# Optimization experiments

Hardware: AMD Instinct MI355X
Metric: run time of the kernel (lower is better)

## Reference

```python
import jax, jax.numpy as jnp
import numpy as np

D_MODEL = 512
D_AUX = 64
B, N = 8, 2048


def setup_inputs() -> dict:
    key = jax.random.key(0)
    ks = jax.random.split(key, 12)
    lim = 1.0 / np.sqrt(D_MODEL)  # torch Linear default init scale
    inp = {
        "x": jax.random.normal(ks[0], (B, N, D_MODEL), dtype=jnp.float32),
        "query_aux": jax.random.normal(ks[1], (B, N, D_AUX), dtype=jnp.float32),
        "key_aux": jax.random.normal(ks[2], (B, N, D_AUX), dtype=jnp.float32),
        "adjacency_mask": jax.random.randint(ks[3], (B, N, N), 0, 2, dtype=jnp.int32),
        "merge_coefficients": jnp.float32(0.3),
        "Wq": jax.random.uniform(ks[4], (D_MODEL, D_MODEL), jnp.float32, -lim, lim),
        "bq": jax.random.uniform(ks[5], (D_MODEL,), jnp.float32, -lim, lim),
        "Wk": jax.random.uniform(ks[6], (D_MODEL, D_MODEL), jnp.float32, -lim, lim),
        "bk": jax.random.uniform(ks[7], (D_MODEL,), jnp.float32, -lim, lim),
        "Wv": jax.random.uniform(ks[8], (D_MODEL, D_MODEL), jnp.float32, -lim, lim),
        "bv": jax.random.uniform(ks[9], (D_MODEL,), jnp.float32, -lim, lim),
        "threshold": jnp.float32(0.5),
    }
    return inp


def reference(x, query_aux, key_aux, adjacency_mask, merge_coefficients,
              Wq, bq, Wk, bk, Wv, bv, threshold):
    d_model = x.shape[-1]
    d_aux = key_aux.shape[-1]
    scale = jnp.asarray(d_model, x.dtype) ** 0.5
    scale_aux = jnp.asarray(d_aux, x.dtype) ** 0.5

    q = x @ Wq.T + bq  # [B,N,D]
    k = x @ Wk.T + bk
    v = x @ Wv.T + bv

    scores = jnp.einsum('bnd,bmd->bnm', q, k) / scale  # [B,N,N]
    scores_aux = jnp.einsum('bnd,bmd->bnm', query_aux, key_aux) / scale_aux

    # data-dependent merge: where aux score nonzero AND score above learned threshold
    merge_mask = (scores_aux != 0) & (scores > threshold)
    merged = (1.0 - merge_coefficients) * scores + merge_coefficients * scores_aux
    scores = jnp.where(merge_mask, merged, scores)

    mask_value = jnp.finfo(scores.dtype).min
    scores = jnp.where(adjacency_mask == 0, mask_value, scores)

    weights = jax.nn.softmax(scores, axis=-1)
    return jnp.einsum('bnm,bmd->bnd', weights, v)
```

## Files before the change

### kernel.cpp

```cpp
#include <hip/hip_runtime.h>
#include <cstdint>

#define SEQ    2048
#define DM     512
#define DAUX   64

typedef _Float16 f16;
typedef __attribute__((ext_vector_type(2))) _Float16 f16x2;
typedef __attribute__((ext_vector_type(4))) _Float16 f16x4;
typedef __attribute__((ext_vector_type(8))) _Float16 f16x8;
typedef __attribute__((ext_vector_type(4))) float fx4;

__device__ __forceinline__ void g2l16(const void* g, void* l) {
  __builtin_amdgcn_global_load_lds(
      (__attribute__((address_space(1))) void*)const_cast<void*>(g),
      (__attribute__((address_space(3))) void*)l, 16, 0, 0);
}

__device__ __forceinline__ void stage64(const f16* __restrict__ g0, int stride,
                                        f16* lds, int t) {
#pragma unroll
  for (int p = 0; p < 4; ++p) {
    int L = p * 256 + t;
    int row = L >> 3;
    int jp = L & 7;
    int jl = jp ^ (row & 7);
    g2l16(g0 + (size_t)row * stride + jl * 8, lds + L * 8);
  }
}

__device__ __forceinline__ f16x8 frag64(const f16* lds, int row, int kq) {
  int jp = (kq >> 3) ^ (row & 7);
  return *(const f16x8*)(lds + row * 64 + jp * 8);
}

__device__ __forceinline__ void chunk3(const f16* Ah, const f16* Al,
                                       const f16* Bh, const f16* Bl,
                                       fx4 acc[4][4], int wm, int wn, int lane) {
  const int r15 = lane & 15;
  const int q8 = (lane >> 4) * 8;
#pragma unroll
  for (int k0 = 0; k0 < 64; k0 += 32) {
    f16x8 ah[4], al[4];
#pragma unroll
    for (int it = 0; it < 4; ++it) {
      int row = wm * 64 + it * 16 + r15;
      ah[it] = frag64(Ah, row, k0 + q8);
      al[it] = frag64(Al, row, k0 + q8);
    }
#pragma unroll
    for (int jt = 0; jt < 4; ++jt) {
      int col = wn * 64 + jt * 16 + r15;
      f16x8 bh = frag64(Bh, col, k0 + q8);
      f16x8 bl = frag64(Bl, col, k0 + q8);
#pragma unroll
      for (int it = 0; it < 4; ++it) {
        acc[it][jt] = __builtin_amdgcn_mfma_f32_16x16x32_f16(ah[it], bh, acc[it][jt], 0, 0, 0);
        acc[it][jt] = __builtin_amdgcn_mfma_f32_16x16x32_f16(ah[it], bl, acc[it][jt], 0, 0, 0);
        acc[it][jt] = __builtin_amdgcn_mfma_f32_16x16x32_f16(al[it], bh, acc[it][jt], 0, 0, 0);
      }
    }
  }
}

__device__ __forceinline__ void chunk1(const f16* A, const f16* B,
                                       fx4 acc[4][4], int wm, int wn, int lane) {
  const int r15 = lane & 15;
  const int q8 = (lane >> 4) * 8;
#pragma unroll
  for (int k0 = 0; k0 < 64; k0 += 32) {
    f16x8 a[4];
#pragma unroll
    for (int it = 0; it < 4; ++it)
      a[it] = frag64(A, wm * 64 + it * 16 + r15, k0 + q8);
#pragma unroll
    for (int jt = 0; jt < 4; ++jt) {
      f16x8 b = frag64(B, wn * 64 + jt * 16 + r15, k0 + q8);
#pragma unroll
      for (int it = 0; it < 4; ++it)
        acc[it][jt] = __builtin_amdgcn_mfma_f32_16x16x32_f16(a[it], b, acc[it][jt], 0, 0, 0);
    }
  }
}

__global__ __launch_bounds__(256) void convert_split(
    const float* __restrict__ x, const float* __restrict__ Wq,
    const float* __restrict__ Wk, const float* __restrict__ Wv,
    f16* __restrict__ xh, f16* __restrict__ xl,
    f16* __restrict__ Wh, f16* __restrict__ Wl) {
  int idx = blockIdx.x * 256 + threadIdx.x;
  const float* src; f16* dh; f16* dl; size_t off;
  if (idx < 2097152) { src = x; off = (size_t)idx; dh = xh; dl = xl; }
  else {
    int rr = idx - 2097152;
    int w = rr >> 16, o = rr & 65535;
    src = (w == 0) ? Wq : (w == 1) ? Wk : Wv;
    off = (size_t)o;
    dh = Wh + (size_t)w * 262144; dl = Wl + (size_t)w * 262144;
  }
  float4 v = ((const float4*)src)[off];
  float vv[4] = {v.x, v.y, v.z, v.w};
  f16x4 hv, lv;
#pragma unroll
  for (int i = 0; i < 4; ++i) {
    float s = vv[i] * 32.0f;
    f16 hi = (f16)s;
    hv[i] = hi;
    lv[i] = (f16)(s - (float)hi);
  }
  *(f16x4*)(dh + off * 4) = hv;
  *(f16x4*)(dl + off * 4) = lv;
}

__global__ __launch_bounds__(256) void qkv_mfma(
    const f16* __restrict__ xh, const f16* __restrict__ xl,
    const f16* __restrict__ Wh, const f16* __restrict__ Wl,
    const float* __restrict__ bq, const float* __restrict__ bk, const float* __restrict__ bv,
    f16* __restrict__ qh, f16* __restrict__ ql,
    f16* __restrict__ kh, f16* __restrict__ kl,
    f16* __restrict__ vt) {
  __shared__ __align__(16) f16 sm[32768];
  f16 *Ah = sm, *Al = sm + 8192, *Bh = sm + 16384, *Bl = sm + 24576;
  const int t = threadIdx.x;
  const int i0 = blockIdx.x * 128, j0 = blockIdx.y * 128, z = blockIdx.z;
  const f16* WhZ = Wh + (size_t)z * 262144;
  const f16* WlZ = Wl + (size_t)z * 262144;
  const int lane = t & 63, wave = t >> 6;
  const int wm = wave >> 1, wn = wave & 1;
  fx4 acc[4][4] = {};
  if (z < 2) {
    for (int d0 = 0; d0 < DM; d0 += 64) {
      __syncthreads();
      stage64(xh + (size_t)i0 * DM + d0, DM, Ah, t);
      stage64(xl + (size_t)i0 * DM + d0, DM, Al, t);
      stage64(WhZ + (size_t)j0 * DM + d0, DM, Bh, t);
      stage64(WlZ + (size_t)j0 * DM + d0, DM, Bl, t);
      __syncthreads();
      chunk3(Ah, Al, Bh, Bl, acc, wm, wn, lane);
    }
  } else {
    for (int d0 = 0; d0 < DM; d0 += 64) {
      __syncthreads();
      stage64(xh + (size_t)i0 * DM + d0, DM, Ah, t);
      stage64(WhZ + (size_t)j0 * DM + d0, DM, Bh, t);
      __syncthreads();
      chunk1(Ah, Bh, acc, wm, wn, lane);
    }
  }
  const float* bias = (z == 0) ? bq : (z == 1) ? bk : bv;
  const int q4 = (lane >> 4) * 4, r15 = lane & 15;
  if (z < 2) {
    f16* oh = z ? kh : qh;  f16* ol = z ? kl : ql;
#pragma unroll
    for (int jt = 0; jt < 4; ++jt) {
      int j = j0 + wn * 64 + jt * 16 + r15;
      float bj = bias[j];
#pragma unroll
      for (int it = 0; it < 4; ++it) {
        int ib = i0 + wm * 64 + it * 16 + q4;
#pragma unroll
        for (int g = 0; g < 4; ++g) {
          float val = acc[it][jt][g] * (1.0f / 1024.0f) + bj;
          float s = val * 32.0f;
          f16 hi = (f16)s;
          oh[(size_t)(ib + g) * DM + j] = hi;
          ol[(size_t)(ib + g) * DM + j] = (f16)(s - (float)hi);
        }
      }
    }
  } else {
#pragma unroll
    for (int jt = 0; jt < 4; ++jt) {
      int j = j0 + wn * 64 + jt * 16 + r15;
      float bj = bias[j];
#pragma unroll
      for (int it = 0; it < 4; ++it) {
        int ib = i0 + wm * 64 + it * 16 + q4;
        int bb = ib >> 11, nb = ib & 2047;
        f16x4 hv;
#pragma unroll
        for (int g = 0; g < 4; ++g)
          hv[g] = (f16)(acc[it][jt][g] * (1.0f / 1024.0f) + bj);
        *(f16x4*)(vt + ((size_t)(bb * DM + j)) * SEQ + nb) = hv;
      }
    }
  }
}

__global__ __launch_bounds__(256) void scores_mfma(
    const f16* __restrict__ qh, const f16* __restrict__ ql,
    const f16* __restrict__ kh, const f16* __restrict__ kl,
    const float* __restrict__ qa, const float* __restrict__ ka,
    const int* __restrict__ adj,
    const float* __restrict__ mc_p, const float* __restrict__ thr_p,
    f16* __restrict__ S16) {
  __shared__ __align__(16) f16 sm[32768];
  f16 *Ah = sm, *Al = sm + 8192, *Bh = sm + 16384, *Bl = sm + 24576;
  f16 *QAl = sm;
  f16 *KAl = sm + 9216;
  const int t = threadIdx.x;
  const int n0 = blockIdx.x * 128, m0 = blockIdx.y * 128, b = blockIdx.z;
  const int lane = t & 63, wave = t >> 6;
  const int wm = wave >> 1, wn = wave & 1;
  const int r15 = lane & 15, qd = lane >> 4;

  const float* QAb = qa + ((size_t)b * SEQ + n0) * DAUX;
  const float* KAb = ka + ((size_t)b * SEQ + m0) * DAUX;
#pragma unroll
  for (int p = 0; p < 4; ++p) {
    int L8 = p * 256 + t;
    int row = L8 >> 3, c8 = (L8 & 7) * 8;
    float4 u0 = *(const float4*)(QAb + (size_t)row * DAUX + c8);
    float4 u1 = *(const float4*)(QAb + (size_t)row * DAUX + c8 + 4);
    f16x8 hq = {(f16)u0.x,(f16)u0.y,(f16)u0.z,(f16)u0.w,(f16)u1.x,(f16)u1.y,(f16)u1.z,(f16)u1.w};
    *(f16x8*)(QAl + row * 72 + c8) = hq;
    float4 w0 = *(const float4*)(KAb + (size_t)row * DAUX + c8);
    float4 w1 = *(const float4*)(KAb + (size_t)row * DAUX + c8 + 4);
    f16x8 hk = {(f16)w0.x,(f16)w0.y,(f16)w0.z,(f16)w0.w,(f16)w1.x,(f16)w1.y,(f16)w1.z,(f16)w1.w};
    *(f16x8*)(KAl + row * 72 + c8) = hk;
  }
  __syncthreads();
  f16x2 sax[4][4][2];
  {
    const int q8 = qd * 8;
    f16x8 qa_f[4][2], ka_f[4][2];
#pragma unroll
    for (int it = 0; it < 4; ++it) {
      int row = wm * 64 + it * 16 + r15;
      qa_f[it][0] = *(const f16x8*)(QAl + row * 72 + q8);
      qa_f[it][1] = *(const f16x8*)(QAl + row * 72 + 32 + q8);
    }
#pragma unroll
    for (int jt = 0; jt < 4; ++jt) {
      int col = wn * 64 + jt * 16 + r15;
      ka_f[jt][0] = *(const f16x8*)(KAl + col * 72 + q8);
      ka_f[jt][1] = *(const f16x8*)(KAl + col * 72 + 32 + q8);
    }
#pragma unroll
    for (int it = 0; it < 4; ++it)
#pragma unroll
      for (int jt = 0; jt < 4; ++jt) {
        fx4 tmp = {0.f, 0.f, 0.f, 0.f};
        tmp = __builtin_amdgcn_mfma_f32_16x16x32_f16(qa_f[it][0], ka_f[jt][0], tmp, 0, 0, 0);
        tmp = __builtin_amdgcn_mfma_f32_16x16x32_f16(qa_f[it][1], ka_f[jt][1], tmp, 0, 0, 0);
        sax[it][jt][0] = f16x2{(f16)tmp[0], (f16)tmp[1]};
        sax[it][jt][1] = f16x2{(f16)tmp[2], (f16)tmp[3]};
      }
  }
  fx4 acc[4][4] = {};
  const f16* qhB = qh + ((size_t)b * SEQ + n0) * DM;
  const f16* qlB = ql + ((size_t)b * SEQ + n0) * DM;
  const f16* khB = kh + ((size_t)b * SEQ + m0) * DM;
  const f16* klB = kl + ((size_t)b * SEQ + m0) * DM;
  for (int d0 = 0; d0 < DM; d0 += 64) {
    __syncthreads();
    stage64(qhB + d0, DM, Ah, t);
    stage64(qlB + d0, DM, Al, t);
    stage64(khB + d0, DM, Bh, t);
    stage64(klB + d0, DM, Bl, t);
    __syncthreads();
    chunk3(Ah, Al, Bh, Bl, acc, wm, wn, lane);
  }
  const float mc = *mc_p, thr = *thr_p;
  const float invC = 1.0f / (1024.0f * 22.62741699796952f);
#pragma unroll
  for (int it = 0; it < 4; ++it) {
    int rowb = n0 + wm * 64 + it * 16 + qd * 4;
#pragma unroll
    for (int g = 0; g < 4; ++g) {
      size_t rbase = ((size_t)b * SEQ + rowb + g) * SEQ;
#pragma unroll
      for (int jt = 0; jt < 4; ++jt) {
        int col = m0 + wn * 64 + jt * 16 + r15;
        float s = acc[it][jt][g] * invC;
        float sa = (float)sax[it][jt][g >> 1][g & 1] * 0.125f;
        if (sa != 0.0f && s > thr) s = (1.0f - mc) * s + mc * sa;
        if (adj[rbase + col] == 0) s = -65504.0f;
        S16[rbase + col] = (f16)s;
      }
    }
  }
}

__global__ __launch_bounds__(256) void softmax_p(
    f16* __restrict__ S16, float* __restrict__ rowsum) {
  const size_t row = blockIdx.x;
  f16* Sr = S16 + row * SEQ;
  const int t = threadIdx.x;
  f16x8 v = *(const f16x8*)(Sr + t * 8);
  float vals[8];
#pragma unroll
  for (int i = 0; i < 8; ++i) vals[i] = (float)v[i];
  float m = vals[0];
#pragma unroll
  for (int i = 1; i < 8; ++i) m = fmaxf(m, vals[i]);
#pragma unroll
  for (int off = 32; off >= 1; off >>= 1) m = fmaxf(m, __shfl_down(m, off, 64));
  __shared__ float wred[4];
  __shared__ float bmax;
  const int wv = t >> 6, ln = t & 63;
  if (ln == 0) wred[wv] = m;
  __syncthreads();
  if (t == 0) bmax = fmaxf(fmaxf(wred[0], wred[1]), fmaxf(wred[2], wred[3]));
  __syncthreads();
  const float mm = bmax;
  f16x8 p16;
  float z = 0.f;
#pragma unroll
  for (int i = 0; i < 8; ++i) {
    f16 p = (f16)(__expf(vals[i] - mm) * 1024.0f);
    p16[i] = p;
    z += (float)p;
  }
#pragma unroll
  for (int off = 32; off >= 1; off >>= 1) z += __shfl_down(z, off, 64);
  __syncthreads();
  if (ln == 0) wred[wv] = z;
  __syncthreads();
  if (t == 0) rowsum[row] = wred[0] + wred[1] + wred[2] + wred[3];
  *(f16x8*)(Sr + t * 8) = p16;
}

__global__ __launch_bounds__(256) void pv_mfma(
    const f16* __restrict__ P16, const f16* __restrict__ vt,
    const float* __restrict__ rowsum, float* __restrict__ O) {
  __shared__ __align__(16) f16 sm[16384];
  f16 *Ps = sm, *Vs = sm + 8192;
  const int t = threadIdx.x;
  const int n0 = blockIdx.x * 128, d0 = blockIdx.y * 128, b = blockIdx.z;
  const int lane = t & 63, wave = t >> 6;
  const int wm = wave >> 1, wn = wave & 1;
  fx4 acc[4][4] = {};
  const f16* Pb = P16 + ((size_t)b * SEQ + n0) * SEQ;
  const f16* Vb = vt + ((size_t)b * DM + d0) * SEQ;
  for (int m0 = 0; m0 < SEQ; m0 += 64) {
    __syncthreads();
    stage64(Pb + m0, SEQ, Ps, t);
    stage64(Vb + m0, SEQ, Vs, t);
    __syncthreads();
    chunk1(Ps, Vs, acc, wm, wn, lane);
  }
  const int r15 = lane & 15, qd = lane >> 4;
#pragma unroll
  for (int it = 0; it < 4; ++it) {
    int nb = n0 + wm * 64 + it * 16 + qd * 4;
#pragma unroll
    for (int g = 0; g < 4; ++g) {
      float inv = 1.0f / rowsum[(size_t)b * SEQ + nb + g];
      size_t obase = ((size_t)b * SEQ + nb + g) * DM;
#pragma unroll
      for (int jt = 0; jt < 4; ++jt) {
        int d = d0 + wn * 64 + jt * 16 + r15;
        O[obase + d] = acc[it][jt][g] * inv;
      }
    }
  }
}

extern "C" void kernel_launch(void* const* d_in, const int* in_sizes, int n_in,
                              void* d_out, int out_size, void* d_ws, size_t ws_size,
                              hipStream_t stream) {
  const float* x   = (const float*)d_in[0];
  const float* qa  = (const float*)d_in[1];
  const float* ka  = (const float*)d_in[2];
  const int*   adj = (const int*)d_in[3];
  const float* mc  = (const float*)d_in[4];
  const float* Wq  = (const float*)d_in[5];
  const float* bq  = (const float*)d_in[6];
  const float* Wk  = (const float*)d_in[7];
  const float* bk  = (const float*)d_in[8];
  const float* Wv  = (const float*)d_in[9];
  const float* bv  = (const float*)d_in[10];
  const float* thr = (const float*)d_in[11];
  float* out = (float*)d_out;

  f16* qh  = (f16*)d_ws;
  f16* ql  = qh + 8388608;
  f16* kh  = ql + 8388608;
  f16* kl  = kh + 8388608;
  f16* vt  = kl + 8388608;
  f16* S16 = vt + 8388608;
  float* rowsum = (float*)(S16 + 33554432);
  f16* xh = S16;
  f16* xl = xh + 8388608;
  f16* Wh = xl + 8388608;
  f16* Wl = Wh + 786432;

  convert_split<<<8960, 256, 0, stream>>>(x, Wq, Wk, Wv, xh, xl, Wh, Wl);
  qkv_mfma<<<dim3(128, 4, 3), 256, 0, stream>>>(xh, xl, Wh, Wl, bq, bk, bv,
                                                qh, ql, kh, kl, vt);
  scores_mfma<<<dim3(16, 16, 8), 256, 0, stream>>>(qh, ql, kh, kl, qa, ka, adj,
                                                   mc, thr, S16);
  softmax_p<<<16384, 256, 0, stream>>>(S16, rowsum);
  pv_mfma<<<dim3(16, 4, 8), 256, 0, stream>>>(S16, vt, rowsum, out);
}
```

Measured before the change: 535.6 us.

## Switch GEMMs to 32x32x16 MFMA tiles and halve LDS K-chunks

Replaces the 16x16x32 MFMA fragments with 32x32x16 instructions in the QKV, scores and PV GEMMs, changing the accumulator layout and epilogue indexing. The split-precision GEMMs now stage 32-wide K chunks with a new swizzle, which halves shared memory per block and may allow more resident blocks. The aim is fewer LDS fragment reads per FLOP and better occupancy. The cost is twice as many sync-separated staging iterations and epilogue stores whose write patterns are less coalesced.

```diff
diff --git a/kernel.cpp b/kernel.cpp
--- a/kernel.cpp
+++ b/kernel.cpp
@@ -10,11 +10,28 @@
 typedef __attribute__((ext_vector_type(4))) _Float16 f16x4;
 typedef __attribute__((ext_vector_type(8))) _Float16 f16x8;
 typedef __attribute__((ext_vector_type(4))) float fx4;
+typedef __attribute__((ext_vector_type(16))) float fx16;
 
 __device__ __forceinline__ void g2l16(const void* g, void* l) {
   __builtin_amdgcn_global_load_lds(
       (__attribute__((address_space(1))) void*)const_cast<void*>(g),
       (__attribute__((address_space(3))) void*)l, 16, 0, 0);
+}
+
+__device__ __forceinline__ void stage32(const f16* __restrict__ g0, int stride,
+                                        f16* lds, int t) {
+#pragma unroll
+  for (int p = 0; p < 2; ++p) {
+    int L = p * 256 + t;
+    int row = L >> 2;
+    int jp = L & 3;
+    int jl = jp ^ ((row >> 1) & 3);
+    g2l16(g0 + (size_t)row * stride + jl * 8, lds + L * 8);
+  }
+}
+__device__ __forceinline__ f16x8 frag32(const f16* lds, int row, int kq) {
+  int jp = (kq >> 3) ^ ((row >> 1) & 3);
+  return *(const f16x8*)(lds + row * 32 + jp * 8);
 }
 
 __device__ __forceinline__ void stage64(const f16* __restrict__ g0, int stride,
@@ -28,57 +45,56 @@
     g2l16(g0 + (size_t)row * stride + jl * 8, lds + L * 8);
   }
 }
-
 __device__ __forceinline__ f16x8 frag64(const f16* lds, int row, int kq) {
   int jp = (kq >> 3) ^ (row & 7);
   return *(const f16x8*)(lds + row * 64 + jp * 8);
 }
 
-__device__ __forceinline__ void chunk3(const f16* Ah, const f16* Al,
-                                       const f16* Bh, const f16* Bl,
-                                       fx4 acc[4][4], int wm, int wn, int lane) {
-  const int r15 = lane & 15;
-  const int q8 = (lane >> 4) * 8;
-#pragma unroll
-  for (int k0 = 0; k0 < 64; k0 += 32) {
-    f16x8 ah[4], al[4];
-#pragma unroll
-    for (int it = 0; it < 4; ++it) {
-      int row = wm * 64 + it * 16 + r15;
-      ah[it] = frag64(Ah, row, k0 + q8);
-      al[it] = frag64(Al, row, k0 + q8);
-    }
-#pragma unroll
-    for (int jt = 0; jt < 4; ++jt) {
-      int col = wn * 64 + jt * 16 + r15;
-      f16x8 bh = frag64(Bh, col, k0 + q8);
-      f16x8 bl = frag64(Bl, col, k0 + q8);
-#pragma unroll
-      for (int it = 0; it < 4; ++it) {
-        acc[it][jt] = __builtin_amdgcn_mfma_f32_16x16x32_f16(ah[it], bh, acc[it][jt], 0, 0, 0);
-        acc[it][jt] = __builtin_amdgcn_mfma_f32_16x16x32_f16(ah[it], bl, acc[it][jt], 0, 0, 0);
-        acc[it][jt] = __builtin_amdgcn_mfma_f32_16x16x32_f16(al[it], bh, acc[it][jt], 0, 0, 0);
-      }
-    }
-  }
-}
-
-__device__ __forceinline__ void chunk1(const f16* A, const f16* B,
-                                       fx4 acc[4][4], int wm, int wn, int lane) {
-  const int r15 = lane & 15;
-  const int q8 = (lane >> 4) * 8;
-#pragma unroll
-  for (int k0 = 0; k0 < 64; k0 += 32) {
-    f16x8 a[4];
-#pragma unroll
-    for (int it = 0; it < 4; ++it)
-      a[it] = frag64(A, wm * 64 + it * 16 + r15, k0 + q8);
-#pragma unroll
-    for (int jt = 0; jt < 4; ++jt) {
-      f16x8 b = frag64(B, wn * 64 + jt * 16 + r15, k0 + q8);
-#pragma unroll
-      for (int it = 0; it < 4; ++it)
-        acc[it][jt] = __builtin_amdgcn_mfma_f32_16x16x32_f16(a[it], b, acc[it][jt], 0, 0, 0);
+__device__ __forceinline__ void chunk3_32(const f16* Ah, const f16* Al,
+                                          const f16* Bh, const f16* Bl,
+                                          fx16 acc[2][2], int wm, int wn, int lane) {
+  const int r31 = lane & 31;
+  const int kq = (lane >> 5) * 8;
+#pragma unroll
+  for (int k0 = 0; k0 < 32; k0 += 16) {
+    f16x8 ah[2], al[2];
+#pragma unroll
+    for (int it = 0; it < 2; ++it) {
+      int row = wm * 64 + it * 32 + r31;
+      ah[it] = frag32(Ah, row, k0 + kq);
+      al[it] = frag32(Al, row, k0 + kq);
+    }
+#pragma unroll
+    for (int jt = 0; jt < 2; ++jt) {
+      int col = wn * 64 + jt * 32 + r31;
+      f16x8 bh = frag32(Bh, col, k0 + kq);
+      f16x8 bl = frag32(Bl, col, k0 + kq);
+#pragma unroll
+      for (int it = 0; it < 2; ++it) {
+        acc[it][jt] = __builtin_amdgcn_mfma_f32_32x32x16_f16(ah[it], bh, acc[it][jt], 0, 0, 0);
+        acc[it][jt] = __builtin_amdgcn_mfma_f32_32x32x16_f16(ah[it], bl, acc[it][jt], 0, 0, 0);
+        acc[it][jt] = __builtin_amdgcn_mfma_f32_32x32x16_f16(al[it], bh, acc[it][jt], 0, 0, 0);
+      }
+    }
+  }
+}
+
+__device__ __forceinline__ void chunk1_64(const f16* A, const f16* B,
+                                          fx16 acc[2][2], int wm, int wn, int lane) {
+  const int r31 = lane & 31;
+  const int kq = (lane >> 5) * 8;
+#pragma unroll
+  for (int k0 = 0; k0 < 64; k0 += 16) {
+    f16x8 a[2];
+#pragma unroll
+    for (int it = 0; it < 2; ++it)
+      a[it] = frag64(A, wm * 64 + it * 32 + r31, k0 + kq);
+#pragma unroll
+    for (int jt = 0; jt < 2; ++jt) {
+      f16x8 b = frag64(B, wn * 64 + jt * 32 + r31, k0 + kq);
+#pragma unroll
+      for (int it = 0; it < 2; ++it)
+        acc[it][jt] = __builtin_amdgcn_mfma_f32_32x32x16_f16(a[it], b, acc[it][jt], 0, 0, 0);
     }
   }
 }
@@ -119,71 +135,73 @@
     f16* __restrict__ qh, f16* __restrict__ ql,
     f16* __restrict__ kh, f16* __restrict__ kl,
     f16* __restrict__ vt) {
-  __shared__ __align__(16) f16 sm[32768];
-  f16 *Ah = sm, *Al = sm + 8192, *Bh = sm + 16384, *Bl = sm + 24576;
+  __shared__ __align__(16) f16 sm[16384];
   const int t = threadIdx.x;
   const int i0 = blockIdx.x * 128, j0 = blockIdx.y * 128, z = blockIdx.z;
   const f16* WhZ = Wh + (size_t)z * 262144;
   const f16* WlZ = Wl + (size_t)z * 262144;
   const int lane = t & 63, wave = t >> 6;
   const int wm = wave >> 1, wn = wave & 1;
-  fx4 acc[4][4] = {};
+  const int r31 = lane & 31, half = lane >> 5;
+  fx16 acc[2][2] = {};
   if (z < 2) {
-    for (int d0 = 0; d0 < DM; d0 += 64) {
+    f16 *Ah = sm, *Al = sm + 4096, *Bh = sm + 8192, *Bl = sm + 12288;
+    for (int d0 = 0; d0 < DM; d0 += 32) {
       __syncthreads();
-      stage64(xh + (size_t)i0 * DM + d0, DM, Ah, t);
-      stage64(xl + (size_t)i0 * DM + d0, DM, Al, t);
-      stage64(WhZ + (size_t)j0 * DM + d0, DM, Bh, t);
-      stage64(WlZ + (size_t)j0 * DM + d0, DM, Bl, t);
+      stage32(xh + (size_t)i0 * DM + d0, DM, Ah, t);
+      stage32(xl + (size_t)i0 * DM + d0, DM, Al, t);
+      stage32(WhZ + (size_t)j0 * DM + d0, DM, Bh, t);
+      stage32(WlZ + (size_t)j0 * DM + d0, DM, Bl, t);
       __syncthreads();
-      chunk3(Ah, Al, Bh, Bl, acc, wm, wn, lane);
+      chunk3_32(Ah, Al, Bh, Bl, acc, wm, wn, lane);
     }
   } else {
+    f16 *Ah = sm, *Bh = sm + 8192;
     for (int d0 = 0; d0 < DM; d0 += 64) {
       __syncthreads();
       stage64(xh + (size_t)i0 * DM + d0, DM, Ah, t);
       stage64(WhZ + (size_t)j0 * DM + d0, DM, Bh, t);
       __syncthreads();
-      chunk1(Ah, Bh, acc, wm, wn, lane);
+      chunk1_64(Ah, Bh, acc, wm, wn, lane);
     }
   }
   const float* bias = (z == 0) ? bq : (z == 1) ? bk : bv;
-  const int q4 = (lane >> 4) * 4, r15 = lane & 15;
   if (z < 2) {
     f16* oh = z ? kh : qh;  f16* ol = z ? kl : ql;
 #pragma unroll
-    for (int jt = 0; jt < 4; ++jt) {
-      int j = j0 + wn * 64 + jt * 16 + r15;
-      float bj = bias[j];
-#pragma unroll
-      for (int it = 0; it < 4; ++it) {
-        int ib = i0 + wm * 64 + it * 16 + q4;
-#pragma unroll
-        for (int g = 0; g < 4; ++g) {
-          float val = acc[it][jt][g] * (1.0f / 1024.0f) + bj;
+    for (int it = 0; it < 2; ++it)
+#pragma unroll
+      for (int jt = 0; jt < 2; ++jt) {
+        int j = j0 + wn * 64 + jt * 32 + r31;
+        float bj = bias[j];
+#pragma unroll
+        for (int r = 0; r < 16; ++r) {
+          int ib = i0 + wm * 64 + it * 32 + (r & 3) + 8 * (r >> 2) + 4 * half;
+          float val = acc[it][jt][r] * (1.0f / 1024.0f) + bj;
           float s = val * 32.0f;
           f16 hi = (f16)s;
-          oh[(size_t)(ib + g) * DM + j] = hi;
-          ol[(size_t)(ib + g) * DM + j] = (f16)(s - (float)hi);
+          oh[(size_t)ib * DM + j] = hi;
+          ol[(size_t)ib * DM + j] = (f16)(s - (float)hi);
         }
       }
-    }
   } else {
 #pragma unroll
-    for (int jt = 0; jt < 4; ++jt) {
-      int j = j0 + wn * 64 + jt * 16 + r15;
-      float bj = bias[j];
-#pragma unroll
-      for (int it = 0; it < 4; ++it) {
-        int ib = i0 + wm * 64 + it * 16 + q4;
-        int bb = ib >> 11, nb = ib & 2047;
-        f16x4 hv;
-#pragma unroll
-        for (int g = 0; g < 4; ++g)
-          hv[g] = (f16)(acc[it][jt][g] * (1.0f / 1024.0f) + bj);
-        *(f16x4*)(vt + ((size_t)(bb * DM + j)) * SEQ + nb) = hv;
-      }
-    }
+    for (int it = 0; it < 2; ++it)
+#pragma unroll
+      for (int jt = 0; jt < 2; ++jt) {
+        int j = j0 + wn * 64 + jt * 32 + r31;
+        float bj = bias[j];
+#pragma unroll
+        for (int q4 = 0; q4 < 4; ++q4) {
+          int ib = i0 + wm * 64 + it * 32 + 8 * q4 + 4 * half;
+          int bb = ib >> 11, nb = ib & 2047;
+          f16x4 hv;
+#pragma unroll
+          for (int g = 0; g < 4; ++g)
+            hv[g] = (f16)(acc[it][jt][q4 * 4 + g] * (1.0f / 1024.0f) + bj);
+          *(f16x4*)(vt + ((size_t)(bb * DM + j)) * SEQ + nb) = hv;
+        }
+      }
   }
 }
 
@@ -194,92 +212,92 @@
     const int* __restrict__ adj,
     const float* __restrict__ mc_p, const float* __restrict__ thr_p,
     f16* __restrict__ S16) {
-  __shared__ __align__(16) f16 sm[32768];
-  f16 *Ah = sm, *Al = sm + 8192, *Bh = sm + 16384, *Bl = sm + 24576;
+  __shared__ __align__(16) f16 sm[16384];
+  f16 *Ah = sm, *Al = sm + 4096, *Bh = sm + 8192, *Bl = sm + 12288;
   f16 *QAl = sm;
-  f16 *KAl = sm + 9216;
+  f16 *KAl = sm + 8192;
   const int t = threadIdx.x;
   const int n0 = blockIdx.x * 128, m0 = blockIdx.y * 128, b = blockIdx.z;
   const int lane = t & 63, wave = t >> 6;
   const int wm = wave >> 1, wn = wave & 1;
-  const int r15 = lane & 15, qd = lane >> 4;
+  const int r31 = lane & 31, half = lane >> 5;
+  const int kq = half * 8;
 
   const float* QAb = qa + ((size_t)b * SEQ + n0) * DAUX;
   const float* KAb = ka + ((size_t)b * SEQ + m0) * DAUX;
 #pragma unroll
   for (int p = 0; p < 4; ++p) {
     int L8 = p * 256 + t;
-    int row = L8 >> 3, c8 = (L8 & 7) * 8;
+    int row = L8 >> 3, jb = L8 & 7;
+    int c8 = jb * 8;
+    int jp = jb ^ (row & 7);
     float4 u0 = *(const float4*)(QAb + (size_t)row * DAUX + c8);
     float4 u1 = *(const float4*)(QAb + (size_t)row * DAUX + c8 + 4);
     f16x8 hq = {(f16)u0.x,(f16)u0.y,(f16)u0.z,(f16)u0.w,(f16)u1.x,(f16)u1.y,(f16)u1.z,(f16)u1.w};
-    *(f16x8*)(QAl + row * 72 + c8) = hq;
+    *(f16x8*)(QAl + row * 64 + jp * 8) = hq;
     float4 w0 = *(const float4*)(KAb + (size_t)row * DAUX + c8);
     float4 w1 = *(const float4*)(KAb + (size_t)row * DAUX + c8 + 4);
     f16x8 hk = {(f16)w0.x,(f16)w0.y,(f16)w0.z,(f16)w0.w,(f16)w1.x,(f16)w1.y,(f16)w1.z,(f16)w1.w};
-    *(f16x8*)(KAl + row * 72 + c8) = hk;
+    *(f16x8*)(KAl + row * 64 + jp * 8) = hk;
   }
   __syncthreads();
-  f16x2 sax[4][4][2];
+  f16x2 sax2[2][2][8];
   {
-    const int q8 = qd * 8;
-    f16x8 qa_f[4][2], ka_f[4][2];
-#pragma unroll
-    for (int it = 0; it < 4; ++it) {
-      int row = wm * 64 + it * 16 + r15;
-      qa_f[it][0] = *(const f16x8*)(QAl + row * 72 + q8);
-      qa_f[it][1] = *(const f16x8*)(QAl + row * 72 + 32 + q8);
-    }
-#pragma unroll
-    for (int jt = 0; jt < 4; ++jt) {
-      int col = wn * 64 + jt * 16 + r15;
-      ka_f[jt][0] = *(const f16x8*)(KAl + col * 72 + q8);
-      ka_f[jt][1] = *(const f16x8*)(KAl + col * 72 + 32 + q8);
-    }
-#pragma unroll
-    for (int it = 0; it < 4; ++it)
-#pragma unroll
-      for (int jt = 0; jt < 4; ++jt) {
-        fx4 tmp = {0.f, 0.f, 0.f, 0.f};
-        tmp = __builtin_amdgcn_mfma_f32_16x16x32_f16(qa_f[it][0], ka_f[jt][0], tmp, 0, 0, 0);
-        tmp = __builtin_amdgcn_mfma_f32_16x16x32_f16(qa_f[it][1], ka_f[jt][1], tmp, 0, 0, 0);
-        sax[it][jt][0] = f16x2{(f16)tmp[0], (f16)tmp[1]};
-        sax[it][jt][1] = f16x2{(f16)tmp[2], (f16)tmp[3]};
-      }
-  }
-  fx4 acc[4][4] = {};
+    fx16 aacc[2][2] = {};
+#pragma unroll
+    for (int k0 = 0; k0 < 64; k0 += 16) {
+      f16x8 qaf[2];
+#pragma unroll
+      for (int it = 0; it < 2; ++it)
+        qaf[it] = frag64(QAl, wm * 64 + it * 32 + r31, k0 + kq);
+#pragma unroll
+      for (int jt = 0; jt < 2; ++jt) {
+        f16x8 kaf = frag64(KAl, wn * 64 + jt * 32 + r31, k0 + kq);
+#pragma unroll
+        for (int it = 0; it < 2; ++it)
+          aacc[it][jt] = __builtin_amdgcn_mfma_f32_32x32x16_f16(qaf[it], kaf, aacc[it][jt], 0, 0, 0);
+      }
+    }
+#pragma unroll
+    for (int it = 0; it < 2; ++it)
+#pragma unroll
+      for (int jt = 0; jt < 2; ++jt)
+#pragma unroll
+        for (int r = 0; r < 16; ++r)
+          sax2[it][jt][r >> 1][r & 1] = (f16)aacc[it][jt][r];
+  }
+  fx16 acc[2][2] = {};
   const f16* qhB = qh + ((size_t)b * SEQ + n0) * DM;
   const f16* qlB = ql + ((size_t)b * SEQ + n0) * DM;
   const f16* khB = kh + ((size_t)b * SEQ + m0) * DM;
   const f16* klB = kl + ((size_t)b * SEQ + m0) * DM;
-  for (int d0 = 0; d0 < DM; d0 += 64) {
+  for (int d0 = 0; d0 < DM; d0 += 32) {
     __syncthreads();
-    stage64(qhB + d0, DM, Ah, t);
-    stage64(qlB + d0, DM, Al, t);
-    stage64(khB + d0, DM, Bh, t);
-    stage64(klB + d0, DM, Bl, t);
+    stage32(qhB + d0, DM, Ah, t);
+    stage32(qlB + d0, DM, Al, t);
+    stage32(khB + d0, DM, Bh, t);
+    stage32(klB + d0, DM, Bl, t);
     __syncthreads();
-    chunk3(Ah, Al, Bh, Bl, acc, wm, wn, lane);
+    chunk3_32(Ah, Al, Bh, Bl, acc, wm, wn, lane);
   }
   const float mc = *mc_p, thr = *thr_p;
   const float invC = 1.0f / (1024.0f * 22.62741699796952f);
 #pragma unroll
-  for (int it = 0; it < 4; ++it) {
-    int rowb = n0 + wm * 64 + it * 16 + qd * 4;
-#pragma unroll
-    for (int g = 0; g < 4; ++g) {
-      size_t rbase = ((size_t)b * SEQ + rowb + g) * SEQ;
-#pragma unroll
-      for (int jt = 0; jt < 4; ++jt) {
-        int col = m0 + wn * 64 + jt * 16 + r15;
-        float s = acc[it][jt][g] * invC;
-        float sa = (float)sax[it][jt][g >> 1][g & 1] * 0.125f;
+  for (int it = 0; it < 2; ++it)
+#pragma unroll
+    for (int jt = 0; jt < 2; ++jt) {
+      int col = m0 + wn * 64 + jt * 32 + r31;
+#pragma unroll
+      for (int r = 0; r < 16; ++r) {
+        int row = n0 + wm * 64 + it * 32 + (r & 3) + 8 * (r >> 2) + 4 * half;
+        size_t rbase = ((size_t)b * SEQ + row) * SEQ;
+        float s = acc[it][jt][r] * invC;
+        float sa = (float)sax2[it][jt][r >> 1][r & 1] * 0.125f;
         if (sa != 0.0f && s > thr) s = (1.0f - mc) * s + mc * sa;
         if (adj[rbase + col] == 0) s = -65504.0f;
         S16[rbase + col] = (f16)s;
       }
     }
-  }
 }
 
 __global__ __launch_bounds__(256) void softmax_p(
@@ -330,7 +348,8 @@
   const int n0 = blockIdx.x * 128, d0 = blockIdx.y * 128, b = blockIdx.z;
   const int lane = t & 63, wave = t >> 6;
   const int wm = wave >> 1, wn = wave & 1;
-  fx4 acc[4][4] = {};
+  const int r31 = lane & 31, half = lane >> 5;
+  fx16 acc[2][2] = {};
   const f16* Pb = P16 + ((size_t)b * SEQ + n0) * SEQ;
   const f16* Vb = vt + ((size_t)b * DM + d0) * SEQ;
   for (int m0 = 0; m0 < SEQ; m0 += 64) {
@@ -338,23 +357,20 @@
     stage64(Pb + m0, SEQ, Ps, t);
     stage64(Vb + m0, SEQ, Vs, t);
     __syncthreads();
-    chunk1(Ps, Vs, acc, wm, wn, lane);
-  }
-  const int r15 = lane & 15, qd = lane >> 4;
-#pragma unroll
-  for (int it = 0; it < 4; ++it) {
-    int nb = n0 + wm * 64 + it * 16 + qd * 4;
-#pragma unroll
-    for (int g = 0; g < 4; ++g) {
-      float inv = 1.0f / rowsum[(size_t)b * SEQ + nb + g];
-      size_t obase = ((size_t)b * SEQ + nb + g) * DM;
-#pragma unroll
-      for (int jt = 0; jt < 4; ++jt) {
-        int d = d0 + wn * 64 + jt * 16 + r15;
-        O[obase + d] = acc[it][jt][g] * inv;
-      }
-    }
-  }
+    chunk1_64(Ps, Vs, acc, wm, wn, lane);
+  }
+#pragma unroll
+  for (int it = 0; it < 2; ++it)
+#pragma unroll
+    for (int jt = 0; jt < 2; ++jt) {
+      int d = d0 + wn * 64 + jt * 32 + r31;
+#pragma unroll
+      for (int r = 0; r < 16; ++r) {
+        int n = n0 + wm * 64 + it * 32 + (r & 3) + 8 * (r >> 2) + 4 * half;
+        float inv = 1.0f / rowsum[(size_t)b * SEQ + n];
+        O[((size_t)b * SEQ + n) * DM + d] = acc[it][jt][r] * inv;
+      }
+    }
 }
 
 extern "C" void kernel_launch(void* const* d_in, const int* in_sizes, int n_in,
```

Measured after the change: 506.8 us. 1.06x faster.
